# Kernel tuning notes

Hardware: AMD Instinct MI355X
Metric: run time of the kernel (lower is better)

The kernel has to match this reference:

```python
import jax, jax.numpy as jnp
import numpy as np

V = 200000      # num_symbols
E = 128         # embed_dim
PAD = V - 1     # padding index
KNN_K = 32
BQ, BS, NN, KT = 2048, 5, 128, 64
D = 2 * E       # d_model
STEPS = 4
H = 2 * D       # LSTMCell hidden


def setup_inputs():
    key = jax.random.key(0)
    ks = jax.random.split(key, 20)
    f = lambda k, s: jax.random.normal(k, s, dtype=jnp.float32) * 0.02
    emb = f(ks[0], (V, E)).at[PAD].set(0.0)  # padding row is zeros
    return dict(
        emb=emb,
        gcn_W=f(ks[1], (E, D)), gcn_wb=jnp.zeros((E,), jnp.float32),
        gate_W=f(ks[2], (1, D)), gate_b=jnp.zeros((1,), jnp.float32),
        se_w1=f(ks[3], (2 * D, D)), se_b1=jnp.zeros((2 * D,), jnp.float32),
        se_w2=f(ks[4], (D, 2 * D)), se_b2=jnp.zeros((D,), jnp.float32),
        ln_g=jnp.ones((D,), jnp.float32), ln_b=jnp.zeros((D,), jnp.float32),
        W_ih=f(ks[5], (4 * H, D)), W_hh=f(ks[6], (4 * H, H)),
        b_ih=jnp.zeros((4 * H,), jnp.float32), b_hh=jnp.zeros((4 * H,), jnp.float32),
        query=jax.random.randint(ks[7], (BQ, 2), 0, V),
        support=jax.random.randint(ks[8], (BS, 2), 0, V),
        q_l_conn=jax.random.randint(ks[9], (BQ, NN, 2), 0, V),
        q_l_deg=jax.random.randint(ks[10], (BQ,), 1, NN),
        q_r_conn=jax.random.randint(ks[11], (BQ, NN, 2), 0, V),
        q_r_deg=jax.random.randint(ks[12], (BQ,), 1, NN),
        s_l_conn=jax.random.randint(ks[13], (BS, NN, 2), 0, V),
        s_l_deg=jax.random.randint(ks[14], (BS,), 1, NN),
        s_r_conn=jax.random.randint(ks[15], (BS, NN, 2), 0, V),
        s_r_deg=jax.random.randint(ks[16], (BS,), 1, NN),
        knn_tab=jax.random.randint(ks[17], (V, KT), 0, V),
    )


def _cos(a, b):
    # F.cosine_similarity with eps=1e-8
    eps = 1e-8
    na = jnp.maximum(jnp.linalg.norm(a, axis=-1), eps)
    nb = jnp.maximum(jnp.linalg.norm(b, axis=-1), eps)
    return jnp.sum(a * b, axis=-1) / (na * nb)


def _neighbor_encoder(conn, eids, emb, gcn_W, gcn_wb, gate_W, gate_b, knn_tab):
    eids = jnp.where((eids < 0) | (eids >= V), PAD, eids)
    rel_e = emb[conn[..., 0]]            # [B,N,E]
    ent_e = emb[conn[..., 1]]            # [B,N,E]
    center = emb[eids][:, None, :]       # [B,1,E]
    # cosine-sim top-k neighbor selection
    sim = _cos(center, ent_e)            # [B,N]
    _, idx = jax.lax.top_k(sim, KNN_K)
    rel_k = jnp.take_along_axis(rel_e, idx[..., None], axis=1)
    ent_k = jnp.take_along_axis(ent_e, idx[..., None], axis=1)
    cat = jnp.concatenate([rel_k, ent_k], axis=-1)         # [B,k,2E]
    structural = jnp.tanh(jnp.mean(cat @ gcn_W.T + gcn_wb, axis=1))  # [B,E]
    # KNN-index branch
    kidx = knn_tab[eids]
    kidx = jnp.where((kidx < 0) | (kidx >= V), PAD, kidx)
    knn_e = emb[kidx]                    # [B,KT,E]
    sim2 = _cos(center, knn_e)
    _, idx2 = jax.lax.top_k(sim2, KNN_K)
    knn_k_e = jnp.take_along_axis(knn_e, idx2[..., None], axis=1)
    pad_rel = jnp.broadcast_to(emb[PAD], knn_k_e.shape)    # pad relation embedding
    cat2 = jnp.concatenate([pad_rel, knn_k_e], axis=-1)
    knn_mean = jnp.tanh(jnp.mean(cat2 @ gcn_W.T + gcn_wb, axis=1))
    # sigmoid gate fusing structural + knn representation
    gate_in = jnp.concatenate([structural, knn_mean], axis=-1)
    alpha = jax.nn.sigmoid(gate_in @ gate_W.T + gate_b)    # [B,1]
    return (1.0 - alpha) * structural + alpha * knn_mean


def _support_enc(x, w1, b1, w2, b2, g, b):
    h = jax.nn.relu(x @ w1.T + b1) @ w2.T + b2 + x
    mu = jnp.mean(h, axis=-1, keepdims=True)
    var = jnp.var(h, axis=-1, keepdims=True)
    return (h - mu) / jnp.sqrt(var + 1e-5) * g + b


def _query_enc(support, query, W_ih, W_hh, b_ih, b_hh):
    # GMatching LSTMCell matching network; support: [1,D], query: [B,D]
    B = query.shape[0]

    def step(carry, _):
        h_r, c = carry
        z = query @ W_ih.T + b_ih + h_r @ W_hh.T + b_hh
        i, f, g, o = jnp.split(z, 4, axis=-1)
        c2 = jax.nn.sigmoid(f) * c + jax.nn.sigmoid(i) * jnp.tanh(g)
        h2 = jax.nn.sigmoid(o) * jnp.tanh(c2)
        h = query + h2[:, :D]
        attn = jax.nn.softmax(h @ support.T, axis=1)       # [B,1]
        r = attn @ support                                  # [B,D]
        return (jnp.concatenate([h, r], axis=1), c2), h

    z0 = jnp.zeros((B, H), query.dtype)
    _, hs = jax.lax.scan(step, (z0, z0), None, length=STEPS)
    return hs[-1]


def reference(emb, gcn_W, gcn_wb, gate_W, gate_b, se_w1, se_b1, se_w2, se_b2,
              ln_g, ln_b, W_ih, W_hh, b_ih, b_hh,
              query, support, q_l_conn, q_l_deg, q_r_conn, q_r_deg,
              s_l_conn, s_l_deg, s_r_conn, s_r_deg, knn_tab):
    ne = lambda conn, eids: _neighbor_encoder(conn, eids, emb, gcn_W, gcn_wb,
                                              gate_W, gate_b, knn_tab)
    ql = ne(q_l_conn, query[:, 0])
    qr = ne(q_r_conn, query[:, 1])
    sl = ne(s_l_conn, support[:, 0])
    sr = ne(s_r_conn, support[:, 1])
    query_n = jnp.concatenate([ql, qr], axis=-1)   # [BQ,D]
    supp_n = jnp.concatenate([sl, sr], axis=-1)    # [BS,D]
    se = lambda x: _support_enc(x, se_w1, se_b1, se_w2, se_b2, ln_g, ln_b)
    support_g = jnp.mean(se(supp_n), axis=0, keepdims=True)   # [1,D]
    query_g = se(query_n)                                      # [BQ,D]
    query_f = _query_enc(support_g, query_g, W_ih, W_hh, b_ih, b_hh)
    qf = query_f / jnp.maximum(jnp.linalg.norm(query_f, axis=-1, keepdims=True), 1e-12)
    sg = support_g / jnp.maximum(jnp.linalg.norm(support_g, axis=-1, keepdims=True), 1e-12)
    return (qf @ sg.T).squeeze(-1)   # [BQ]
```

## Files before the change

### kernel.cpp

```cpp
#include <hip/hip_runtime.h>

#define Vn 200000
#define PADI 199999

typedef unsigned short ushort_t;
typedef unsigned int uint_t;
typedef __attribute__((ext_vector_type(8))) short short8;
typedef __attribute__((ext_vector_type(4))) float float4v;

__device__ __forceinline__ float sigm(float x) { return 1.f / (1.f + expf(-x)); }
__device__ __forceinline__ float dot4(float4 a, float4 b) {
  return a.x*b.x + a.y*b.y + a.z*b.z + a.w*b.w;
}
__device__ __forceinline__ ushort_t f2bf(float x) {
  uint_t u = __float_as_uint(x);
  uint_t r = (u + 0x7fffu + ((u >> 16) & 1u)) >> 16;
  return (ushort_t)r;
}
__device__ __forceinline__ float bf2f(ushort_t h) { return __uint_as_float(((uint_t)h) << 16); }

__device__ __forceinline__ float2 block_reduce2(float a, float b, float2* red) {
  #pragma unroll
  for (int off = 32; off; off >>= 1) { a += __shfl_down(a, off); b += __shfl_down(b, off); }
  __syncthreads();
  if ((threadIdx.x & 63) == 0) red[threadIdx.x >> 6] = make_float2(a, b);
  __syncthreads();
  float2 r;
  r.x = red[0].x + red[1].x + red[2].x + red[3].x;
  r.y = red[0].y + red[1].y + red[2].y + red[3].y;
  return r;
}

__global__ __launch_bounds__(256) void transpose_kernel(
    const float* __restrict__ in, float* __restrict__ out, int R, int Cfull, int c0, int Ct) {
  int idx = blockIdx.x * 256 + threadIdx.x;
  if (idx >= R * Ct) return;
  int c = idx / R, r = idx - c * R;
  out[idx] = in[(size_t)r * Cfull + c0 + c];
}

__global__ __launch_bounds__(256) void build_b2t_kernel(
    const float* __restrict__ W, ushort_t* __restrict__ b2t, int strideK) {
  int n = blockIdx.x, k = threadIdx.x;
  float v = W[(size_t)n*strideK + k];
  ushort_t hi = f2bf(v);
  ushort_t lo = f2bf(v - bf2f(hi));
  ushort_t* row = b2t + (size_t)n*768;
  row[k] = hi; row[256 + k] = hi; row[512 + k] = lo;
}

__global__ __launch_bounds__(256) void bias_sum_kernel(
    const float* __restrict__ a, const float* __restrict__ b, float* __restrict__ o) {
  int i = blockIdx.x*256 + threadIdx.x;
  o[i] = a[i] + b[i];
}

__global__ __launch_bounds__(256) void gemm_bf16_kernel(
    const ushort_t* __restrict__ A2, const ushort_t* __restrict__ B2T,
    float* __restrict__ C, const float* __restrict__ addmat,
    const float* __restrict__ cv, int ldc) {
  __shared__ ushort_t As[128*40];
  __shared__ ushort_t Bs[128*40];
  int t = threadIdx.x;
  int m0 = blockIdx.y * 128, n0 = blockIdx.x * 128;
  int wid = t >> 6, lane = t & 63;
  int wm = (wid >> 1) * 64, wn = (wid & 1) * 64;
  int q = lane >> 4, fr = lane & 15;
  float4v acc[4][4];
  #pragma unroll
  for (int i = 0; i < 4; ++i)
    #pragma unroll
    for (int j = 0; j < 4; ++j) acc[i][j] = (float4v)0.f;

  for (int k0 = 0; k0 < 768; k0 += 32) {
    #pragma unroll
    for (int rnd = 0; rnd < 2; ++rnd) {
      int idx = rnd*256 + t;
      int row = idx >> 2, ch = idx & 3;
      *(short8*)&As[row*40 + ch*8] = *(const short8*)(A2 + (size_t)(m0+row)*768 + k0 + ch*8);
      *(short8*)&Bs[row*40 + ch*8] = *(const short8*)(B2T + (size_t)(n0+row)*768 + k0 + ch*8);
    }
    __syncthreads();
    short8 af[4], bg[4];
    #pragma unroll
    for (int tm = 0; tm < 4; ++tm) af[tm] = *(const short8*)&As[(wm + tm*16 + fr)*40 + q*8];
    #pragma unroll
    for (int tn = 0; tn < 4; ++tn) bg[tn] = *(const short8*)&Bs[(wn + tn*16 + fr)*40 + q*8];
    #pragma unroll
    for (int tm = 0; tm < 4; ++tm)
      #pragma unroll
      for (int tn = 0; tn < 4; ++tn)
        acc[tm][tn] = __builtin_amdgcn_mfma_f32_16x16x32_bf16(af[tm], bg[tn], acc[tm][tn], 0, 0, 0);
    __syncthreads();
  }

  #pragma unroll
  for (int tm = 0; tm < 4; ++tm) {
    int gm = m0 + wm + tm*16 + q*4;
    #pragma unroll
    for (int tn = 0; tn < 4; ++tn) {
      int gn = n0 + wn + tn*16 + fr;
      float cvv = cv ? cv[gn] : 0.f;
      #pragma unroll
      for (int reg = 0; reg < 4; ++reg) {
        size_t off = (size_t)(gm + reg) * ldc + gn;
        float x = acc[tm][tn][reg] + cvv;
        if (addmat) x += addmat[off];
        C[off] = x;
      }
    }
  }
}

__global__ __launch_bounds__(256) void enc_kernel(
    const float* __restrict__ emb, const float* __restrict__ gcnW, const float* __restrict__ gcnb,
    const float* __restrict__ gateW, const float* __restrict__ gateb,
    const int* __restrict__ knn_tab,
    const int* __restrict__ query, const int* __restrict__ support,
    const int* __restrict__ qlc, const int* __restrict__ qrc,
    const int* __restrict__ slc, const int* __restrict__ src,
    float* __restrict__ xbuf) {
  __shared__ float center[128];
  __shared__ float sims[128];
  __shared__ float sims2[64];
  __shared__ int idr[128], ide[128];
  __shared__ int kidxs[64];
  __shared__ int sel[32], sel2[32];
  __shared__ int cnt1, cnt2;
  __shared__ float catbuf[256];
  __shared__ float knnA[128], knnB[128];
  __shared__ float part1[256], part2[256];
  __shared__ float structural[128], knnm[128];
  __shared__ float2 red2[4];

  int t = threadIdx.x;
  int g = blockIdx.x;
  int eid; const int* conn; float* outp;
  if (g < 2048)      { eid = query[2*g];                 conn = qlc + (size_t)g*256;      outp = xbuf + (size_t)g*256; }
  else if (g < 4096) { int b = g-2048; eid = query[2*b+1];  conn = qrc + (size_t)b*256;   outp = xbuf + (size_t)b*256 + 128; }
  else if (g < 4101) { int b = g-4096; eid = support[2*b];  conn = slc + (size_t)b*256;   outp = xbuf + (size_t)(2048+b)*256; }
  else               { int b = g-4101; eid = support[2*b+1]; conn = src + (size_t)b*256;  outp = xbuf + (size_t)(2048+b)*256 + 128; }
  if (eid < 0 || eid >= Vn) eid = PADI;

  if (t == 0) { cnt1 = 0; cnt2 = 0; }
  if (t < 128) {
    int2 cc = ((const int2*)conn)[t];
    idr[t] = cc.x; ide[t] = cc.y;
    center[t] = emb[(size_t)eid*128 + t];
  } else if (t < 192) {
    int kk = knn_tab[(size_t)eid*64 + (t-128)];
    kidxs[t-128] = (kk < 0 || kk >= Vn) ? PADI : kk;
  }
  __syncthreads();

  int gid = t >> 4, ll = t & 15;
  float4 cen0 = *(const float4*)&center[ll*8];
  float4 cen1 = *(const float4*)&center[ll*8 + 4];
  float cn2 = dot4(cen0, cen0) + dot4(cen1, cen1);
  #pragma unroll
  for (int off = 8; off; off >>= 1) cn2 += __shfl_down(cn2, off, 16);
  cn2 = __shfl(cn2, 0, 16);
  float cn = fmaxf(sqrtf(cn2), 1e-8f);

  #pragma unroll 2
  for (int it = 0; it < 4; ++it) {
    int n0 = it*32 + gid*2;
    int e0 = ide[n0], e1 = ide[n0+1];
    const float4* p0 = (const float4*)(emb + (size_t)e0*128);
    const float4* p1 = (const float4*)(emb + (size_t)e1*128);
    float4 a0 = p0[ll*2], b0 = p0[ll*2+1];
    float4 a1 = p1[ll*2], b1 = p1[ll*2+1];
    float d0 = dot4(a0, cen0) + dot4(b0, cen1), m0 = dot4(a0, a0) + dot4(b0, b0);
    float d1 = dot4(a1, cen0) + dot4(b1, cen1), m1 = dot4(a1, a1) + dot4(b1, b1);
    #pragma unroll
    for (int off = 8; off; off >>= 1) {
      d0 += __shfl_down(d0, off, 16); m0 += __shfl_down(m0, off, 16);
      d1 += __shfl_down(d1, off, 16); m1 += __shfl_down(m1, off, 16);
    }
    if (ll == 0) {
      sims[n0]   = d0 / (cn * fmaxf(sqrtf(m0), 1e-8f));
      sims[n0+1] = d1 / (cn * fmaxf(sqrtf(m1), 1e-8f));
    }
  }
  #pragma unroll 2
  for (int it = 0; it < 2; ++it) {
    int n0 = it*32 + gid*2;
    int e0 = kidxs[n0], e1 = kidxs[n0+1];
    const float4* p0 = (const float4*)(emb + (size_t)e0*128);
    const float4* p1 = (const float4*)(emb + (size_t)e1*128);
    float4 a0 = p0[ll*2], b0 = p0[ll*2+1];
    float4 a1 = p1[ll*2], b1 = p1[ll*2+1];
    float d0 = dot4(a0, cen0) + dot4(b0, cen1), m0 = dot4(a0, a0) + dot4(b0, b0);
    float d1 = dot4(a1, cen0) + dot4(b1, cen1), m1 = dot4(a1, a1) + dot4(b1, b1);
    #pragma unroll
    for (int off = 8; off; off >>= 1) {
      d0 += __shfl_down(d0, off, 16); m0 += __shfl_down(m0, off, 16);
      d1 += __shfl_down(d1, off, 16); m1 += __shfl_down(m1, off, 16);
    }
    if (ll == 0) {
      sims2[n0]   = d0 / (cn * fmaxf(sqrtf(m0), 1e-8f));
      sims2[n0+1] = d1 / (cn * fmaxf(sqrtf(m1), 1e-8f));
    }
  }
  __syncthreads();

  if (t < 128) {
    float my = sims[t];
    int c = 0;
    for (int j = 0; j < 128; ++j) {
      float sj = sims[j];
      c += (sj > my) || (sj == my && j < t);
    }
    if (c < 32) { int p = atomicAdd(&cnt1, 1); sel[p] = t; }
  } else if (t < 192) {
    int i = t - 128;
    float my = sims2[i];
    int c = 0;
    for (int j = 0; j < 64; ++j) {
      float sj = sims2[j];
      c += (sj > my) || (sj == my && j < i);
    }
    if (c < 32) { int p = atomicAdd(&cnt2, 1); sel2[p] = i; }
  }
  __syncthreads();

  {
    int i = t & 127;
    float a0 = 0.f, a1 = 0.f, a2 = 0.f, a3 = 0.f;
    float k0 = 0.f, k1 = 0.f;
    if (t < 128) {
      #pragma unroll 2
      for (int k = 0; k < 32; k += 4) {
        a0 += emb[(size_t)idr[sel[k+0]]*128 + i];
        a1 += emb[(size_t)idr[sel[k+1]]*128 + i];
        a2 += emb[(size_t)idr[sel[k+2]]*128 + i];
        a3 += emb[(size_t)idr[sel[k+3]]*128 + i];
      }
      catbuf[i] = (a0+a1+a2+a3) * (1.f/32.f);
      #pragma unroll 2
      for (int k = 0; k < 16; k += 2) {
        k0 += emb[(size_t)kidxs[sel2[k+0]]*128 + i];
        k1 += emb[(size_t)kidxs[sel2[k+1]]*128 + i];
      }
      knnA[i] = k0 + k1;
    } else {
      #pragma unroll 2
      for (int k = 0; k < 32; k += 4) {
        a0 += emb[(size_t)ide[sel[k+0]]*128 + i];
        a1 += emb[(size_t)ide[sel[k+1]]*128 + i];
        a2 += emb[(size_t)ide[sel[k+2]]*128 + i];
        a3 += emb[(size_t)ide[sel[k+3]]*128 + i];
      }
      catbuf[128 + i] = (a0+a1+a2+a3) * (1.f/32.f);
      #pragma unroll 2
      for (int k = 16; k < 32; k += 2) {
        k0 += emb[(size_t)kidxs[sel2[k+0]]*128 + i];
        k1 += emb[(size_t)kidxs[sel2[k+1]]*128 + i];
      }
      knnB[i] = k0 + k1;
    }
  }
  __syncthreads();

  {
    int i = t & 127, half = t >> 7;
    const float4* w1p = (const float4*)(gcnW + (size_t)i*256 + half*128);
    const float4* c1p = (const float4*)(catbuf + half*128);
    float p1 = 0.f;
    #pragma unroll 8
    for (int j = 0; j < 32; ++j) {
      float4 w = w1p[j], a = c1p[j];
      p1 += dot4(w, a);
    }
    const float4* w2p = (const float4*)(gcnW + (size_t)i*256 + 128 + half*64);
    const float4* kap = (const float4*)(knnA + half*64);
    const float4* kbp = (const float4*)(knnB + half*64);
    float p2 = 0.f;
    #pragma unroll 8
    for (int j = 0; j < 16; ++j) {
      float4 w = w2p[j], xa = kap[j], xb = kbp[j];
      float4 s = make_float4(xa.x+xb.x, xa.y+xb.y, xa.z+xb.z, xa.w+xb.w);
      p2 += dot4(w, s);
    }
    part1[t] = p1;
    part2[t] = p2 * (1.f/32.f);
  }
  __syncthreads();
  if (t < 128) {
    structural[t] = tanhf(part1[t] + part1[t+128] + gcnb[t]);
    knnm[t]       = tanhf(part2[t] + part2[t+128] + gcnb[t]);
  }
  __syncthreads();

  float gv = (t < 128) ? structural[t]*gateW[t] : knnm[t-128]*gateW[t];
  float2 rr = block_reduce2(gv, 0.f, red2);
  float alpha = sigm(rr.x + gateb[0]);
  if (t < 128) outp[t] = (1.f - alpha)*structural[t] + alpha*knnm[t];
}

__global__ __launch_bounds__(256) void qenc_kernel(
    const float* __restrict__ xin, const float* __restrict__ w1t, const float* __restrict__ b1,
    const float* __restrict__ w2t, const float* __restrict__ b2,
    const float* __restrict__ lng, const float* __restrict__ lnb,
    float* __restrict__ xout, ushort_t* __restrict__ a2) {
  __shared__ float xs[8][256];
  __shared__ float hsm[8][512];
  __shared__ float2 red2[4];
  int t = threadIdx.x;
  int r0 = blockIdx.x * 8;
  #pragma unroll
  for (int rr = 0; rr < 8; ++rr) xs[rr][t] = xin[(size_t)(r0+rr)*256 + t];
  __syncthreads();
  #pragma unroll
  for (int uo = 0; uo < 512; uo += 256) {
    int u = uo + t;
    float bv = b1[u];
    float acc[8];
    #pragma unroll
    for (int rr = 0; rr < 8; ++rr) acc[rr] = bv;
    for (int j4 = 0; j4 < 64; ++j4) {
      float w0 = w1t[(size_t)(j4*4+0)*512 + u];
      float w1v = w1t[(size_t)(j4*4+1)*512 + u];
      float w2v = w1t[(size_t)(j4*4+2)*512 + u];
      float w3 = w1t[(size_t)(j4*4+3)*512 + u];
      #pragma unroll
      for (int rr = 0; rr < 8; ++rr) {
        float4 x = *(const float4*)&xs[rr][j4*4];
        acc[rr] += x.x*w0 + x.y*w1v + x.z*w2v + x.w*w3;
      }
    }
    #pragma unroll
    for (int rr = 0; rr < 8; ++rr) hsm[rr][u] = fmaxf(acc[rr], 0.f);
  }
  __syncthreads();
  float val[8];
  {
    float bv = b2[t];
    #pragma unroll
    for (int rr = 0; rr < 8; ++rr) val[rr] = bv + xs[rr][t];
    for (int u4 = 0; u4 < 128; ++u4) {
      float w0 = w2t[(size_t)(u4*4+0)*256 + t];
      float w1v = w2t[(size_t)(u4*4+1)*256 + t];
      float w2v = w2t[(size_t)(u4*4+2)*256 + t];
      float w3 = w2t[(size_t)(u4*4+3)*256 + t];
      #pragma unroll
      for (int rr = 0; rr < 8; ++rr) {
        float4 h4 = *(const float4*)&hsm[rr][u4*4];
        val[rr] += h4.x*w0 + h4.y*w1v + h4.z*w2v + h4.w*w3;
      }
    }
  }
  float gv = lng[t], bv2 = lnb[t];
  for (int rr = 0; rr < 8; ++rr) {
    int r = r0 + rr;
    float2 sq = block_reduce2(val[rr], val[rr]*val[rr], red2);
    float mu  = sq.x * (1.f/256.f);
    float var = sq.y * (1.f/256.f) - mu*mu;
    float rs  = 1.f / sqrtf(var + 1e-5f);
    float ov  = (val[rr] - mu) * rs * gv + bv2;
    xout[(size_t)r*256 + t] = ov;
    if (r < 2048) {
      ushort_t hi = f2bf(ov);
      ushort_t lo = f2bf(ov - bf2f(hi));
      ushort_t* row = a2 + (size_t)r*768;
      row[t] = hi; row[256 + t] = lo; row[512 + t] = hi;
    }
  }
}

__global__ __launch_bounds__(256) void finalize_kernel(
    const float* __restrict__ qout, const float* __restrict__ whh,
    float* __restrict__ sg_hat, float* __restrict__ z_supp) {
  __shared__ float sg[256];
  __shared__ float2 red2[4];
  int t = threadIdx.x;
  float acc = 0.f;
  #pragma unroll
  for (int s = 0; s < 5; ++s) acc += qout[(size_t)(2048+s)*256 + t];
  float sgv = acc * 0.2f;
  sg[t] = sgv;
  float2 nn = block_reduce2(sgv*sgv, 0.f, red2);
  if (blockIdx.x == 0) sg_hat[t] = sgv / fmaxf(sqrtf(nn.x), 1e-12f);
  __syncthreads();
  int u = blockIdx.x*256 + t;
  const float4* w4 = (const float4*)(whh + (size_t)u*512 + 256);
  float a = 0.f;
  #pragma unroll 4
  for (int j4 = 0; j4 < 64; ++j4) {
    float4 wv = w4[j4];
    float4 sv = *(const float4*)&sg[j4*4];
    a += dot4(wv, sv);
  }
  z_supp[u] = a;
}

__global__ __launch_bounds__(256) void gate_kernel(
    const float* __restrict__ Z, const float* __restrict__ qg,
    float* __restrict__ c, ushort_t* __restrict__ a2, int step0) {
  int idx = blockIdx.x * 256 + threadIdx.x;
  int r = idx >> 9, j = idx & 511;
  const float* zr = Z + (size_t)r * 1792;
  float zi = zr[j], zf = zr[512 + j], zg = zr[1024 + j];
  float cold = step0 ? 0.f : c[idx];
  float c2 = sigm(zf) * cold + sigm(zi) * tanhf(zg);
  c[idx] = c2;
  if (j < 256) {
    float zo = zr[1536 + j];
    float h = qg[(size_t)r*256 + j] + sigm(zo) * tanhf(c2);
    ushort_t hi = f2bf(h);
    ushort_t lo = f2bf(h - bf2f(hi));
    ushort_t* row = a2 + (size_t)r*768;
    row[j] = hi; row[256 + j] = lo; row[512 + j] = hi;
  }
}

__global__ __launch_bounds__(256) void gatecos_kernel(
    const float* __restrict__ Z, const float* __restrict__ qg, const float* __restrict__ c,
    const float* __restrict__ sgh, float* __restrict__ out) {
  int wid = threadIdx.x >> 6, lane = threadIdx.x & 63;
  int r = blockIdx.x*4 + wid;
  const float* zr = Z + (size_t)r * 1792;
  float d = 0.f, n2 = 0.f;
  #pragma unroll
  for (int i = 0; i < 4; ++i) {
    int j = lane + i*64;
    float zi = zr[j], zf = zr[512 + j], zg = zr[1024 + j], zo = zr[1536 + j];
    float cold = c[(size_t)r*512 + j];
    float c2 = sigm(zf) * cold + sigm(zi) * tanhf(zg);
    float h = qg[(size_t)r*256 + j] + sigm(zo) * tanhf(c2);
    d += h * sgh[j];
    n2 += h * h;
  }
  #pragma unroll
  for (int off = 32; off; off >>= 1) { d += __shfl_down(d, off); n2 += __shfl_down(n2, off); }
  if (lane == 0) out[r] = d / fmaxf(sqrtf(n2), 1e-12f);
}

extern "C" void kernel_launch(void* const* d_in, const int* in_sizes, int n_in,
                              void* d_out, int out_size, void* d_ws, size_t ws_size,
                              hipStream_t stream) {
  const float* emb   = (const float*)d_in[0];
  const float* gcnW  = (const float*)d_in[1];
  const float* gcnb  = (const float*)d_in[2];
  const float* gateW = (const float*)d_in[3];
  const float* gateb = (const float*)d_in[4];
  const float* sew1  = (const float*)d_in[5];
  const float* seb1  = (const float*)d_in[6];
  const float* sew2  = (const float*)d_in[7];
  const float* seb2  = (const float*)d_in[8];
  const float* lng   = (const float*)d_in[9];
  const float* lnb   = (const float*)d_in[10];
  const float* Wih   = (const float*)d_in[11];
  const float* Whh   = (const float*)d_in[12];
  const float* bih   = (const float*)d_in[13];
  const float* bhh   = (const float*)d_in[14];
  const int* query   = (const int*)d_in[15];
  const int* support = (const int*)d_in[16];
  const int* qlc     = (const int*)d_in[17];
  const int* qrc     = (const int*)d_in[19];
  const int* slc     = (const int*)d_in[21];
  const int* src     = (const int*)d_in[23];
  const int* knn     = (const int*)d_in[25];
  float* out = (float*)d_out;

  float* w = (float*)d_ws;
  size_t o = 0;
  auto alloc = [&](size_t n) { float* p = w + o; o += (n + 15) & ~(size_t)15; return p; };
  float* xbuf      = alloc((size_t)2056*256);
  float* query_g   = alloc((size_t)2056*256);
  float* sg_hat    = alloc(256);
  float* z_supp    = alloc(1792);
  float* cbuf      = alloc((size_t)2048*512);
  float* Abuf      = alloc((size_t)2048*1792);
  float* Zbuf      = alloc((size_t)2048*1792);
  float* w1t       = alloc(256*512);
  float* w2t       = alloc(512*256);
  float* bias_s    = alloc(1792);
  ushort_t* A2     = (ushort_t*)alloc((size_t)2048*768/2);
  ushort_t* B2ih   = (ushort_t*)alloc((size_t)1792*768/2);
  ushort_t* B2hh   = (ushort_t*)alloc((size_t)1792*768/2);
  (void)ws_size; (void)in_sizes; (void)n_in; (void)out_size;

  transpose_kernel<<<512,  256, 0, stream>>>(sew1, w1t, 512, 256, 0, 256);
  transpose_kernel<<<1024, 256, 0, stream>>>(sew2, w2t, 256, 512, 0, 512);
  build_b2t_kernel<<<1792, 256, 0, stream>>>(Wih, B2ih, 256);
  build_b2t_kernel<<<1792, 256, 0, stream>>>(Whh, B2hh, 512);
  bias_sum_kernel<<<7, 256, 0, stream>>>(bih, bhh, bias_s);

  enc_kernel<<<4106, 256, 0, stream>>>(emb, gcnW, gcnb, gateW, gateb, knn,
                                       query, support, qlc, qrc, slc, src, xbuf);

  qenc_kernel<<<257, 256, 0, stream>>>(xbuf, w1t, seb1, w2t, seb2, lng, lnb, query_g, A2);

  finalize_kernel<<<7, 256, 0, stream>>>(query_g, Whh, sg_hat, z_supp);

  gemm_bf16_kernel<<<dim3(14,16), 256, 0, stream>>>(A2, B2ih, Abuf, nullptr, bias_s, 1792);
  gate_kernel<<<4096, 256, 0, stream>>>(Abuf, query_g, cbuf, A2, 1);
  for (int s = 1; s < 4; ++s) {
    gemm_bf16_kernel<<<dim3(14,16), 256, 0, stream>>>(A2, B2hh, Zbuf, Abuf, z_supp, 1792);
    if (s < 3) gate_kernel<<<4096, 256, 0, stream>>>(Zbuf, query_g, cbuf, A2, 0);
    else       gatecos_kernel<<<512, 256, 0, stream>>>(Zbuf, query_g, cbuf, sg_hat, out);
  }
}
```

Before: 581.8 us.

## Switch LSTM GEMMs from split-bf16 to single fp16, fuse prep kernels

Replaces the three-term bf16 hi/lo split (K=768) with a single fp16 operand (K=256), so each recurrent GEMM does a third of the MFMA work and moves a third of the A/B bytes. The five weight-prep kernels are merged into one launch. The encoder's neighbour and kNN similarity loops are fused into one loop over 192 rows with four rows per group. The last step's GEMM skips column tiles not needed by gatecos. The risk is lower accuracy, since fp16 with one term is less precise than the compensated bf16 split.

New measurement: 534.3 us. 8.2% less time.

```diff
diff --git a/kernel.cpp b/kernel.cpp
--- a/kernel.cpp
+++ b/kernel.cpp
@@ -6,18 +6,16 @@
 typedef unsigned short ushort_t;
 typedef unsigned int uint_t;
 typedef __attribute__((ext_vector_type(8))) short short8;
+typedef _Float16 h8v __attribute__((ext_vector_type(8)));
 typedef __attribute__((ext_vector_type(4))) float float4v;
 
 __device__ __forceinline__ float sigm(float x) { return 1.f / (1.f + expf(-x)); }
 __device__ __forceinline__ float dot4(float4 a, float4 b) {
   return a.x*b.x + a.y*b.y + a.z*b.z + a.w*b.w;
 }
-__device__ __forceinline__ ushort_t f2bf(float x) {
-  uint_t u = __float_as_uint(x);
-  uint_t r = (u + 0x7fffu + ((u >> 16) & 1u)) >> 16;
-  return (ushort_t)r;
-}
-__device__ __forceinline__ float bf2f(ushort_t h) { return __uint_as_float(((uint_t)h) << 16); }
+__device__ __forceinline__ ushort_t f2h(float x) {
+  return __builtin_bit_cast(ushort_t, (_Float16)x);
+}
 
 __device__ __forceinline__ float2 block_reduce2(float a, float b, float2* red) {
   #pragma unroll
@@ -31,84 +29,31 @@
   return r;
 }
 
-__global__ __launch_bounds__(256) void transpose_kernel(
-    const float* __restrict__ in, float* __restrict__ out, int R, int Cfull, int c0, int Ct) {
-  int idx = blockIdx.x * 256 + threadIdx.x;
-  if (idx >= R * Ct) return;
-  int c = idx / R, r = idx - c * R;
-  out[idx] = in[(size_t)r * Cfull + c0 + c];
-}
-
-__global__ __launch_bounds__(256) void build_b2t_kernel(
-    const float* __restrict__ W, ushort_t* __restrict__ b2t, int strideK) {
-  int n = blockIdx.x, k = threadIdx.x;
-  float v = W[(size_t)n*strideK + k];
-  ushort_t hi = f2bf(v);
-  ushort_t lo = f2bf(v - bf2f(hi));
-  ushort_t* row = b2t + (size_t)n*768;
-  row[k] = hi; row[256 + k] = hi; row[512 + k] = lo;
-}
-
-__global__ __launch_bounds__(256) void bias_sum_kernel(
-    const float* __restrict__ a, const float* __restrict__ b, float* __restrict__ o) {
-  int i = blockIdx.x*256 + threadIdx.x;
-  o[i] = a[i] + b[i];
-}
-
-__global__ __launch_bounds__(256) void gemm_bf16_kernel(
-    const ushort_t* __restrict__ A2, const ushort_t* __restrict__ B2T,
-    float* __restrict__ C, const float* __restrict__ addmat,
-    const float* __restrict__ cv, int ldc) {
-  __shared__ ushort_t As[128*40];
-  __shared__ ushort_t Bs[128*40];
-  int t = threadIdx.x;
-  int m0 = blockIdx.y * 128, n0 = blockIdx.x * 128;
-  int wid = t >> 6, lane = t & 63;
-  int wm = (wid >> 1) * 64, wn = (wid & 1) * 64;
-  int q = lane >> 4, fr = lane & 15;
-  float4v acc[4][4];
-  #pragma unroll
-  for (int i = 0; i < 4; ++i)
-    #pragma unroll
-    for (int j = 0; j < 4; ++j) acc[i][j] = (float4v)0.f;
-
-  for (int k0 = 0; k0 < 768; k0 += 32) {
-    #pragma unroll
-    for (int rnd = 0; rnd < 2; ++rnd) {
-      int idx = rnd*256 + t;
-      int row = idx >> 2, ch = idx & 3;
-      *(short8*)&As[row*40 + ch*8] = *(const short8*)(A2 + (size_t)(m0+row)*768 + k0 + ch*8);
-      *(short8*)&Bs[row*40 + ch*8] = *(const short8*)(B2T + (size_t)(n0+row)*768 + k0 + ch*8);
-    }
-    __syncthreads();
-    short8 af[4], bg[4];
-    #pragma unroll
-    for (int tm = 0; tm < 4; ++tm) af[tm] = *(const short8*)&As[(wm + tm*16 + fr)*40 + q*8];
-    #pragma unroll
-    for (int tn = 0; tn < 4; ++tn) bg[tn] = *(const short8*)&Bs[(wn + tn*16 + fr)*40 + q*8];
-    #pragma unroll
-    for (int tm = 0; tm < 4; ++tm)
-      #pragma unroll
-      for (int tn = 0; tn < 4; ++tn)
-        acc[tm][tn] = __builtin_amdgcn_mfma_f32_16x16x32_bf16(af[tm], bg[tn], acc[tm][tn], 0, 0, 0);
-    __syncthreads();
-  }
-
-  #pragma unroll
-  for (int tm = 0; tm < 4; ++tm) {
-    int gm = m0 + wm + tm*16 + q*4;
-    #pragma unroll
-    for (int tn = 0; tn < 4; ++tn) {
-      int gn = n0 + wn + tn*16 + fr;
-      float cvv = cv ? cv[gn] : 0.f;
-      #pragma unroll
-      for (int reg = 0; reg < 4; ++reg) {
-        size_t off = (size_t)(gm + reg) * ldc + gn;
-        float x = acc[tm][tn][reg] + cvv;
-        if (addmat) x += addmat[off];
-        C[off] = x;
-      }
-    }
+__global__ __launch_bounds__(256) void prep_kernel(
+    const float* __restrict__ sew1, const float* __restrict__ sew2,
+    const float* __restrict__ Wih, const float* __restrict__ Whh,
+    const float* __restrict__ bih, const float* __restrict__ bhh,
+    float* __restrict__ w1t, float* __restrict__ w2t,
+    ushort_t* __restrict__ Bih, ushort_t* __restrict__ Bhh,
+    float* __restrict__ bias_s) {
+  int b = blockIdx.x, t = threadIdx.x;
+  if (b < 512) {
+    int idx = b*256 + t;
+    int c = idx >> 9, r = idx & 511;
+    w1t[idx] = sew1[(size_t)r*256 + c];
+  } else if (b < 1024) {
+    int idx = (b-512)*256 + t;
+    int c = idx >> 8, r = idx & 255;
+    w2t[idx] = sew2[(size_t)r*512 + c];
+  } else if (b < 2816) {
+    int n = b - 1024;
+    Bih[(size_t)n*256 + t] = f2h(Wih[(size_t)n*256 + t]);
+  } else if (b < 4608) {
+    int n = b - 2816;
+    Bhh[(size_t)n*256 + t] = f2h(Whh[(size_t)n*512 + t]);
+  } else {
+    int i = (b-4608)*256 + t;
+    if (i < 1792) bias_s[i] = bih[i] + bhh[i];
   }
 }
 
@@ -121,8 +66,7 @@
     const int* __restrict__ slc, const int* __restrict__ src,
     float* __restrict__ xbuf) {
   __shared__ float center[128];
-  __shared__ float sims[128];
-  __shared__ float sims2[64];
+  __shared__ float simsu[192];
   __shared__ int idr[128], ide[128];
   __shared__ int kidxs[64];
   __shared__ int sel[32], sel2[32];
@@ -162,62 +106,53 @@
   cn2 = __shfl(cn2, 0, 16);
   float cn = fmaxf(sqrtf(cn2), 1e-8f);
 
-  #pragma unroll 2
-  for (int it = 0; it < 4; ++it) {
-    int n0 = it*32 + gid*2;
-    int e0 = ide[n0], e1 = ide[n0+1];
-    const float4* p0 = (const float4*)(emb + (size_t)e0*128);
-    const float4* p1 = (const float4*)(emb + (size_t)e1*128);
-    float4 a0 = p0[ll*2], b0 = p0[ll*2+1];
-    float4 a1 = p1[ll*2], b1 = p1[ll*2+1];
-    float d0 = dot4(a0, cen0) + dot4(b0, cen1), m0 = dot4(a0, a0) + dot4(b0, b0);
-    float d1 = dot4(a1, cen0) + dot4(b1, cen1), m1 = dot4(a1, a1) + dot4(b1, b1);
+  #pragma unroll
+  for (int it = 0; it < 3; ++it) {
+    int rbase = it*64 + gid*4;
+    int e[4];
+    #pragma unroll
+    for (int rr = 0; rr < 4; ++rr) {
+      int n = rbase + rr;
+      e[rr] = (n < 128) ? ide[n] : kidxs[n-128];
+    }
+    float d[4], m[4];
+    #pragma unroll
+    for (int rr = 0; rr < 4; ++rr) {
+      const float4* p = (const float4*)(emb + (size_t)e[rr]*128);
+      float4 a = p[ll*2], bb = p[ll*2+1];
+      d[rr] = dot4(a, cen0) + dot4(bb, cen1);
+      m[rr] = dot4(a, a) + dot4(bb, bb);
+    }
     #pragma unroll
     for (int off = 8; off; off >>= 1) {
-      d0 += __shfl_down(d0, off, 16); m0 += __shfl_down(m0, off, 16);
-      d1 += __shfl_down(d1, off, 16); m1 += __shfl_down(m1, off, 16);
+      #pragma unroll
+      for (int rr = 0; rr < 4; ++rr) {
+        d[rr] += __shfl_down(d[rr], off, 16);
+        m[rr] += __shfl_down(m[rr], off, 16);
+      }
     }
     if (ll == 0) {
-      sims[n0]   = d0 / (cn * fmaxf(sqrtf(m0), 1e-8f));
-      sims[n0+1] = d1 / (cn * fmaxf(sqrtf(m1), 1e-8f));
-    }
-  }
-  #pragma unroll 2
-  for (int it = 0; it < 2; ++it) {
-    int n0 = it*32 + gid*2;
-    int e0 = kidxs[n0], e1 = kidxs[n0+1];
-    const float4* p0 = (const float4*)(emb + (size_t)e0*128);
-    const float4* p1 = (const float4*)(emb + (size_t)e1*128);
-    float4 a0 = p0[ll*2], b0 = p0[ll*2+1];
-    float4 a1 = p1[ll*2], b1 = p1[ll*2+1];
-    float d0 = dot4(a0, cen0) + dot4(b0, cen1), m0 = dot4(a0, a0) + dot4(b0, b0);
-    float d1 = dot4(a1, cen0) + dot4(b1, cen1), m1 = dot4(a1, a1) + dot4(b1, b1);
-    #pragma unroll
-    for (int off = 8; off; off >>= 1) {
-      d0 += __shfl_down(d0, off, 16); m0 += __shfl_down(m0, off, 16);
-      d1 += __shfl_down(d1, off, 16); m1 += __shfl_down(m1, off, 16);
-    }
-    if (ll == 0) {
-      sims2[n0]   = d0 / (cn * fmaxf(sqrtf(m0), 1e-8f));
-      sims2[n0+1] = d1 / (cn * fmaxf(sqrtf(m1), 1e-8f));
+      #pragma unroll
+      for (int rr = 0; rr < 4; ++rr)
+        simsu[rbase+rr] = d[rr] / (cn * fmaxf(sqrtf(m[rr]), 1e-8f));
     }
   }
   __syncthreads();
 
   if (t < 128) {
-    float my = sims[t];
+    float my = simsu[t];
     int c = 0;
     for (int j = 0; j < 128; ++j) {
-      float sj = sims[j];
+      float sj = simsu[j];
       c += (sj > my) || (sj == my && j < t);
     }
     if (c < 32) { int p = atomicAdd(&cnt1, 1); sel[p] = t; }
   } else if (t < 192) {
     int i = t - 128;
-    float my = sims2[i];
+    float my = simsu[128 + i];
     int c = 0;
     for (int j = 0; j < 64; ++j) {
-      float sj = sims2[j];
+      float sj = simsu[128 + j];
       c += (sj > my) || (sj == my && j < i);
     }
     if (c < 32) { int p = atomicAdd(&cnt2, 1); sel2[p] = i; }
@@ -302,7 +237,7 @@
     const float* __restrict__ xin, const float* __restrict__ w1t, const float* __restrict__ b1,
     const float* __restrict__ w2t, const float* __restrict__ b2,
     const float* __restrict__ lng, const float* __restrict__ lnb,
-    float* __restrict__ xout, ushort_t* __restrict__ a2) {
+    float* __restrict__ xout, ushort_t* __restrict__ Ah) {
   __shared__ float xs[8][256];
   __shared__ float hsm[8][512];
   __shared__ float2 red2[4];
@@ -350,21 +285,16 @@
       }
     }
   }
-  float gv = lng[t], bv2 = lnb[t];
+  float gvv = lng[t], bv2 = lnb[t];
   for (int rr = 0; rr < 8; ++rr) {
     int r = r0 + rr;
     float2 sq = block_reduce2(val[rr], val[rr]*val[rr], red2);
     float mu  = sq.x * (1.f/256.f);
     float var = sq.y * (1.f/256.f) - mu*mu;
     float rs  = 1.f / sqrtf(var + 1e-5f);
-    float ov  = (val[rr] - mu) * rs * gv + bv2;
+    float ov  = (val[rr] - mu) * rs * gvv + bv2;
     xout[(size_t)r*256 + t] = ov;
-    if (r < 2048) {
-      ushort_t hi = f2bf(ov);
-      ushort_t lo = f2bf(ov - bf2f(hi));
-      ushort_t* row = a2 + (size_t)r*768;
-      row[t] = hi; row[256 + t] = lo; row[512 + t] = hi;
-    }
+    if (r < 2048) Ah[(size_t)r*256 + t] = f2h(ov);
   }
 }
 
@@ -394,9 +324,70 @@
   z_supp[u] = a;
 }
 
+__global__ __launch_bounds__(256) void gemm_f16_kernel(
+    const ushort_t* __restrict__ A, const ushort_t* __restrict__ BT,
+    float* __restrict__ C, const float* __restrict__ addmat,
+    const float* __restrict__ cv, int remap) {
+  __shared__ ushort_t As[128*40];
+  __shared__ ushort_t Bs[128*40];
+  int t = threadIdx.x;
+  int bx = blockIdx.x;
+  if (remap) bx = (bx >> 1)*4 + (bx & 1);
+  int m0 = blockIdx.y * 128, n0 = bx * 128;
+  int wid = t >> 6, lane = t & 63;
+  int wm = (wid >> 1) * 64, wn = (wid & 1) * 64;
+  int q = lane >> 4, fr = lane & 15;
+  float4v acc[4][4];
+  #pragma unroll
+  for (int i = 0; i < 4; ++i)
+    #pragma unroll
+    for (int j = 0; j < 4; ++j) acc[i][j] = (float4v)0.f;
+
+  for (int k0 = 0; k0 < 256; k0 += 32) {
+    #pragma unroll
+    for (int rnd = 0; rnd < 2; ++rnd) {
+      int idx = rnd*256 + t;
+      int row = idx >> 2, ch = idx & 3;
+      *(short8*)&As[row*40 + ch*8] = *(const short8*)(A + (size_t)(m0+row)*256 + k0 + ch*8);
+      *(short8*)&Bs[row*40 + ch*8] = *(const short8*)(BT + (size_t)(n0+row)*256 + k0 + ch*8);
+    }
+    __syncthreads();
+    short8 af[4], bg[4];
+    #pragma unroll
+    for (int tm = 0; tm < 4; ++tm) af[tm] = *(const short8*)&As[(wm + tm*16 + fr)*40 + q*8];
+    #pragma unroll
+    for (int tn = 0; tn < 4; ++tn) bg[tn] = *(const short8*)&Bs[(wn + tn*16 + fr)*40 + q*8];
+    #pragma unroll
+    for (int tm = 0; tm < 4; ++tm)
+      #pragma unroll
+      for (int tn = 0; tn < 4; ++tn)
+        acc[tm][tn] = __builtin_amdgcn_mfma_f32_16x16x32_f16(
+            __builtin_bit_cast(h8v, af[tm]), __builtin_bit_cast(h8v, bg[tn]),
+            acc[tm][tn], 0, 0, 0);
+    __syncthreads();
+  }
+
+  #pragma unroll
+  for (int tm = 0; tm < 4; ++tm) {
+    int gm = m0 + wm + tm*16 + q*4;
+    #pragma unroll
+    for (int tn = 0; tn < 4; ++tn) {
+      int gn = n0 + wn + tn*16 + fr;
+      float cvv = cv ? cv[gn] : 0.f;
+      #pragma unroll
+      for (int reg = 0; reg < 4; ++reg) {
+        size_t off = (size_t)(gm + reg) * 1792 + gn;
+        float x = acc[tm][tn][reg] + cvv;
+        if (addmat) x += addmat[off];
+        C[off] = x;
+      }
+    }
+  }
+}
+
 __global__ __launch_bounds__(256) void gate_kernel(
     const float* __restrict__ Z, const float* __restrict__ qg,
-    float* __restrict__ c, ushort_t* __restrict__ a2, int step0) {
+    float* __restrict__ c, ushort_t* __restrict__ Ah, int step0) {
   int idx = blockIdx.x * 256 + threadIdx.x;
   int r = idx >> 9, j = idx & 511;
   const float* zr = Z + (size_t)r * 1792;
@@ -407,10 +398,7 @@
   if (j < 256) {
     float zo = zr[1536 + j];
     float h = qg[(size_t)r*256 + j] + sigm(zo) * tanhf(c2);
-    ushort_t hi = f2bf(h);
-    ushort_t lo = f2bf(h - bf2f(hi));
-    ushort_t* row = a2 + (size_t)r*768;
-    row[j] = hi; row[256 + j] = lo; row[512 + j] = hi;
+    Ah[(size_t)r*256 + j] = f2h(h);
   }
 }
 
@@ -469,36 +457,37 @@
   float* xbuf      = alloc((size_t)2056*256);
   float* query_g   = alloc((size_t)2056*256);
   float* sg_hat    = alloc(256);
-  float* z_supp    = alloc(1792);
+  float* z_supp    = alloc(2048);
   float* cbuf      = alloc((size_t)2048*512);
   float* Abuf      = alloc((size_t)2048*1792);
   float* Zbuf      = alloc((size_t)2048*1792);
   float* w1t       = alloc(256*512);
   float* w2t       = alloc(512*256);
-  float* bias_s    = alloc(1792);
-  ushort_t* A2     = (ushort_t*)alloc((size_t)2048*768/2);
-  ushort_t* B2ih   = (ushort_t*)alloc((size_t)1792*768/2);
-  ushort_t* B2hh   = (ushort_t*)alloc((size_t)1792*768/2);
+  float* bias_s    = alloc(2048);
+  ushort_t* Ah     = (ushort_t*)alloc((size_t)2048*128);
+  ushort_t* Bih    = (ushort_t*)alloc((size_t)1792*128);
+  ushort_t* Bhh    = (ushort_t*)alloc((size_t)1792*128);
   (void)ws_size; (void)in_sizes; (void)n_in; (void)out_size;
 
-  transpose_kernel<<<512,  256, 0, stream>>>(sew1, w1t, 512, 256, 0, 256);
-  transpose_kernel<<<1024, 256, 0, stream>>>(sew2, w2t, 256, 512, 0, 512);
-  build_b2t_kernel<<<1792, 256, 0, stream>>>(Wih, B2ih, 256);
-  build_b2t_kernel<<<1792, 256, 0, stream>>>(Whh, B2hh, 512);
-  bias_sum_kernel<<<7, 256, 0, stream>>>(bih, bhh, bias_s);
+  prep_kernel<<<4615, 256, 0, stream>>>(sew1, sew2, Wih, Whh, bih, bhh,
+                                        w1t, w2t, Bih, Bhh, bias_s);
 
   enc_kernel<<<4106, 256, 0, stream>>>(emb, gcnW, gcnb, gateW, gateb, knn,
                                        query, support, qlc, qrc, slc, src, xbuf);
 
-  qenc_kernel<<<257, 256, 0, stream>>>(xbuf, w1t, seb1, w2t, seb2, lng, lnb, query_g, A2);
+  qenc_kernel<<<257, 256, 0, stream>>>(xbuf, w1t, seb1, w2t, seb2, lng, lnb, query_g, Ah);
 
   finalize_kernel<<<7, 256, 0, stream>>>(query_g, Whh, sg_hat, z_supp);
 
-  gemm_bf16_kernel<<<dim3(14,16), 256, 0, stream>>>(A2, B2ih, Abuf, nullptr, bias_s, 1792);
-  gate_kernel<<<4096, 256, 0, stream>>>(Abuf, query_g, cbuf, A2, 1);
+  gemm_f16_kernel<<<dim3(14,16), 256, 0, stream>>>(Ah, Bih, Abuf, nullptr, bias_s, 0);
+  gate_kernel<<<4096, 256, 0, stream>>>(Abuf, query_g, cbuf, Ah, 1);
   for (int s = 1; s < 4; ++s) {
-    gemm_bf16_kernel<<<dim3(14,16), 256, 0, stream>>>(A2, B2hh, Zbuf, Abuf, z_supp, 1792);
-    if (s < 3) gate_kernel<<<4096, 256, 0, stream>>>(Zbuf, query_g, cbuf, A2, 0);
-    else       gatecos_kernel<<<512, 256, 0, stream>>>(Zbuf, query_g, cbuf, sg_hat, out);
-  }
-}
+    if (s < 3) {
+      gemm_f16_kernel<<<dim3(14,16), 256, 0, stream>>>(Ah, Bhh, Zbuf, Abuf, z_supp, 0);
+      gate_kernel<<<4096, 256, 0, stream>>>(Zbuf, query_g, cbuf, Ah, 0);
+    } else {
+      gemm_f16_kernel<<<dim3(8,16), 256, 0, stream>>>(Ah, Bhh, Zbuf, Abuf, z_supp, 1);
+      gatecos_kernel<<<512, 256, 0, stream>>>(Zbuf, query_g, cbuf, sg_hat, out);
+    }
+  }
+}
```
